# Kernel tuning notes

Hardware: AMD Instinct MI355X
Metric: run time of the kernel (lower is better)

## Reference

```python
import jax, jax.numpy as jnp
import numpy as np

DIM = 1024
NUM_EXPERTS = 8
TOP_K = 2
HIDDEN = DIM * 2
B, S = 2, 4096


def setup_inputs() -> dict:
    key = jax.random.key(0)
    ks = jax.random.split(key, 8)
    sd = 1.0 / np.sqrt(DIM)
    sh = 1.0 / np.sqrt(HIDDEN)
    return {
        "x": jax.random.normal(ks[0], (B, S, DIM), dtype=jnp.float32),
        "gate_w": jax.random.uniform(ks[1], (NUM_EXPERTS, DIM), jnp.float32, -sd, sd),
        "gate_b": jax.random.uniform(ks[2], (NUM_EXPERTS,), jnp.float32, -sd, sd),
        "W1": jax.random.uniform(ks[3], (NUM_EXPERTS, DIM, HIDDEN), jnp.float32, -sd, sd),
        "b1": jax.random.uniform(ks[4], (NUM_EXPERTS, HIDDEN), jnp.float32, -sd, sd),
        "W2": jax.random.uniform(ks[5], (NUM_EXPERTS, HIDDEN, DIM), jnp.float32, -sh, sh),
        "b2": jax.random.uniform(ks[6], (NUM_EXPERTS, DIM), jnp.float32, -sh, sh),
    }


def reference(x, gate_w, gate_b, W1, b1, W2, b2):
    Bd, Sd, D = x.shape
    xf = x.reshape(-1, D)                                  # [T, D]
    T = xf.shape[0]
    logits = xf @ gate_w.T + gate_b                        # [T, E]
    weights = jax.nn.softmax(logits.astype(jnp.float32), axis=-1)
    topk_w, topk_i = jax.lax.top_k(weights, TOP_K)         # [T, K]
    topk_w = topk_w / topk_w.sum(axis=-1, keepdims=True)
    # combine weights scattered back to dense [T, E] (top-k indices are distinct)
    comb = jnp.zeros((T, NUM_EXPERTS), topk_w.dtype)
    comb = comb.at[jnp.arange(T)[:, None], topk_i].add(topk_w)
    # dense all-expert FFN (exact GELU, matching nn.GELU default)
    h = jax.nn.gelu(jnp.einsum('td,edh->eth', xf, W1) + b1[:, None, :], approximate=False)
    y = jnp.einsum('eth,ehd->etd', h, W2) + b2[:, None, :]  # [E, T, D]
    out = jnp.einsum('etd,te->td', y, comb.astype(y.dtype)).reshape(Bd, Sd, D)
    return out, logits
```

## Files before the change

### kernel.cpp

```cpp
#include <hip/hip_runtime.h>
#include <math.h>

#define T_TOK 8192
#define DIMX 1024
#define NE 8
#define HID 2048
#define NPAIR (T_TOK * 2)
#define P_PAD (NPAIR + NE * 128)
#define GATE_TPB 32

typedef __attribute__((ext_vector_type(8))) short s16x8;
typedef __attribute__((ext_vector_type(4))) float f32x4;

static __device__ __forceinline__ unsigned short f2bf(float f) {
    union { float f; unsigned u; } v; v.f = f;
    unsigned r = v.u + 0x7FFFu + ((v.u >> 16) & 1u);
    return (unsigned short)(r >> 16);
}
static __device__ __forceinline__ float bf2f(unsigned short u) {
    union { unsigned u; float f; } v; v.u = (unsigned)u << 16; return v.f;
}

static __device__ __forceinline__ float gelu_fast(float v) {
    float u2 = -1.5957691216057308f * v * (1.f + 0.044715f * v * v);
    return v * __builtin_amdgcn_rcpf(1.f + __expf(u2));
}

static __device__ __forceinline__ void gload16(const unsigned short* g, unsigned short* l) {
    __builtin_amdgcn_global_load_lds(
        (const __attribute__((address_space(1))) unsigned int*)g,
        (__attribute__((address_space(3))) unsigned int*)l, 16, 0, 0);
}

__global__ __launch_bounds__(256) void conv_transpose2_kernel(
    const float* __restrict__ W1, const float* __restrict__ W2,
    unsigned short* __restrict__ W1t, unsigned short* __restrict__ W2t, int* counts) {
    __shared__ float tile[64][65];
    int z = blockIdx.z;
    int e = z & 7;
    if (z == 0 && blockIdx.x == 0 && blockIdx.y == 0 && threadIdx.x < NE)
        counts[threadIdx.x] = 0;
    const float* srcb; unsigned short* dstb; int R, C;
    if (z < 8) { srcb = W1; dstb = W1t; R = DIMX; C = HID; }
    else       { srcb = W2; dstb = W2t; R = HID; C = DIMX; }
    int r0 = blockIdx.y * 64, c0 = blockIdx.x * 64;
    if (r0 >= R || c0 >= C) return;
    const float* s = srcb + (size_t)e * R * C;
    unsigned short* d = dstb + (size_t)e * R * C;
    int tid = threadIdx.x;
    int lr = tid >> 4, lc4 = (tid & 15) * 4;
    #pragma unroll
    for (int it = 0; it < 4; it++) {
        float4 v = *(const float4*)&s[(size_t)(r0 + it * 16 + lr) * C + c0 + lc4];
        tile[it * 16 + lr][lc4 + 0] = v.x;
        tile[it * 16 + lr][lc4 + 1] = v.y;
        tile[it * 16 + lr][lc4 + 2] = v.z;
        tile[it * 16 + lr][lc4 + 3] = v.w;
    }
    __syncthreads();
    int cc = tid >> 3, rch = (tid & 7) * 8;
    #pragma unroll
    for (int it = 0; it < 2; it++) {
        int c = it * 32 + cc;
        unsigned short r[8];
        #pragma unroll
        for (int j = 0; j < 8; j++) r[j] = f2bf(tile[rch + j][c]);
        *(uint4*)&d[(size_t)(c0 + c) * R + r0 + rch] = *(const uint4*)&r[0];
    }
}

__global__ __launch_bounds__(256) void gate_kernel(
    const float* __restrict__ x, const float* __restrict__ gw, const float* __restrict__ gb,
    float* __restrict__ logits_out, int* counts, int* __restrict__ pair_epos,
    float* __restrict__ pair_w, unsigned short* __restrict__ xb) {
    __shared__ float sgw[NE * DIMX];
    __shared__ int lcount[NE], lbase[NE];
    __shared__ int s_e[GATE_TPB * 2];
    __shared__ int s_lp[GATE_TPB * 2];
    __shared__ float s_wv[GATE_TPB * 2];
    int tid = threadIdx.x;
    for (int i = tid; i < NE * DIMX / 4; i += 256)
        ((float4*)sgw)[i] = ((const float4*)gw)[i];
    if (tid < NE) lcount[tid] = 0;
    __syncthreads();

    int wave = tid >> 6, lane = tid & 63;
    int tbase = blockIdx.x * GATE_TPB;
    for (int r = 0; r < GATE_TPB / 4; ++r) {
        int ti = wave * (GATE_TPB / 4) + r;
        int t = tbase + ti;
        const float* xr = x + (size_t)t * DIMX;
        float acc[NE] = {};
        #pragma unroll
        for (int i = 0; i < DIMX / 256; i++) {
            float4 xv = *(const float4*)&xr[i * 256 + lane * 4];
            unsigned short rb[4] = { f2bf(xv.x), f2bf(xv.y), f2bf(xv.z), f2bf(xv.w) };
            *(uint2*)&xb[(size_t)t * DIMX + i * 256 + lane * 4] = *(const uint2*)&rb[0];
            #pragma unroll
            for (int e = 0; e < NE; e++) {
                float4 wv = *(const float4*)&sgw[e * DIMX + i * 256 + lane * 4];
                acc[e] += xv.x * wv.x + xv.y * wv.y + xv.z * wv.z + xv.w * wv.w;
            }
        }
        #pragma unroll
        for (int e = 0; e < NE; e++) {
            #pragma unroll
            for (int off = 32; off; off >>= 1) acc[e] += __shfl_xor(acc[e], off);
        }
        if (lane == 0) {
            float* lo = logits_out + (size_t)t * NE;
            #pragma unroll
            for (int e = 0; e < NE; e++) { acc[e] += gb[e]; lo[e] = acc[e]; }
            float l0 = acc[0]; int e0 = 0;
            #pragma unroll
            for (int e = 1; e < NE; e++) if (acc[e] > l0) { l0 = acc[e]; e0 = e; }
            float l1 = -1e30f; int e1 = -1;
            #pragma unroll
            for (int e = 0; e < NE; e++) if (e != e0 && acc[e] > l1) { l1 = acc[e]; e1 = e; }
            float q = expf(l1 - l0);
            float wn0 = 1.f / (1.f + q);
            float wn1 = q / (1.f + q);
            int lp0 = atomicAdd(&lcount[e0], 1);
            int lp1 = atomicAdd(&lcount[e1], 1);
            s_e[ti * 2] = e0; s_lp[ti * 2] = lp0; s_wv[ti * 2] = wn0;
            s_e[ti * 2 + 1] = e1; s_lp[ti * 2 + 1] = lp1; s_wv[ti * 2 + 1] = wn1;
        }
    }
    __syncthreads();
    if (tid < NE) lbase[tid] = atomicAdd(&counts[tid], lcount[tid]);
    __syncthreads();
    if (tid < GATE_TPB * 2) {
        int e = s_e[tid];
        int gp = lbase[e] + s_lp[tid];
        int gi = (tbase + (tid >> 1)) * 2 + (tid & 1);
        pair_epos[gi] = (e << 28) | gp;
        pair_w[gi] = s_wv[tid];
    }
}

__global__ __launch_bounds__(256) void place_kernel(
    const int* __restrict__ pair_epos, const float* __restrict__ pair_w,
    const int* __restrict__ counts, int* __restrict__ offsets_out,
    int* __restrict__ slot_token, float* __restrict__ slot_weight,
    int* __restrict__ tok2slot) {
    __shared__ int soff[NE + 1];
    __shared__ int scnt[NE];
    int tid = threadIdx.x;
    if (tid == 0) {
        int o = 0;
        soff[0] = 0;
        for (int e = 0; e < NE; e++) {
            int c = counts[e];
            scnt[e] = c;
            o += (c + 127) & ~127;
            soff[e + 1] = o;
        }
    }
    __syncthreads();
    if (blockIdx.x == 0 && tid <= NE) offsets_out[tid] = soff[tid];

    int gtid = blockIdx.x * 256 + tid;
    {
        int gbase = 0;
        #pragma unroll
        for (int e = 0; e < NE; e++) {
            int gs = soff[e] + scnt[e];
            int gl = soff[e + 1] - gs;
            int idx = gtid - gbase;
            if (idx >= 0 && idx < gl) {
                slot_token[gs + idx] = 0;
                slot_weight[gs + idx] = 0.f;
            }
            gbase += gl;
        }
    }
    int p = gtid;
    if (p >= NPAIR) return;
    int ep = pair_epos[p];
    int e = ep >> 28;
    int pos = ep & 0x0FFFFFFF;
    int slot = soff[e] + pos;
    slot_token[slot] = p >> 1;
    slot_weight[slot] = pair_w[p];
    tok2slot[p] = slot;
}

#define BARRIER() asm volatile("s_barrier" ::: "memory")
#define WAIT_VM(n) asm volatile("s_waitcnt vmcnt(" #n ")" ::: "memory")
#define WAIT_LGKM0() do { asm volatile("s_waitcnt lgkmcnt(0)" ::: "memory"); \
                          __builtin_amdgcn_sched_barrier(0); } while (0)


__global__ __launch_bounds__(512, 4) void gemm1_kernel(
    const unsigned short* __restrict__ xb, const unsigned short* __restrict__ W1t,
    const float* __restrict__ b1, const int* __restrict__ offsets,
    const int* __restrict__ slot_token, unsigned short* __restrict__ hbuf) {
    int e = blockIdx.x;
    int row_base = offsets[e];
    int rows = offsets[e + 1] - row_base;
    int m0 = blockIdx.z * 128;
    if (m0 >= rows) return;
    int n0 = blockIdx.y * 128;

    __shared__ unsigned short sA[2][128 * 64];
    __shared__ unsigned short sB[2][128 * 64];

    int tid = threadIdx.x;
    const unsigned short* w1e = W1t + (size_t)e * HID * DIMX;

    int srow = tid >> 3;
    int kperm = (tid & 7) ^ (srow & 7);
    int tok0 = slot_token[row_base + m0 + srow];
    int tok1 = slot_token[row_base + m0 + srow + 64];
    const unsigned short* gA0 = xb + (size_t)tok0 * DIMX + kperm * 8;
    const unsigned short* gA1 = xb + (size_t)tok1 * DIMX + kperm * 8;
    const unsigned short* gB0 = w1e + (size_t)(n0 + srow) * DIMX + kperm * 8;
    const unsigned short* gB1 = w1e + (size_t)(n0 + srow + 64) * DIMX + kperm * 8;

#define STG1(b, k0) do { \
        gload16(gA0 + (k0), &sA[b][tid * 8]); \
        gload16(gA1 + (k0), &sA[b][(tid + 512) * 8]); \
        gload16(gB0 + (k0), &sB[b][tid * 8]); \
        gload16(gB1 + (k0), &sB[b][(tid + 512) * 8]); \
    } while (0)

    f32x4 acc[4][2] = {};
    int wid = tid >> 6; int wr = wid >> 2, wc = wid & 3;
    int lane = tid & 63; int lr = lane & 15, lg = lane >> 4;
    int kx0 = lg ^ (lr & 7);

#define CMP1(CUR) do { \
        _Pragma("unroll") \
        for (int kk = 0; kk < 2; kk++) { \
            int kxo = (kx0 ^ (kk * 4)) * 8; \
            s16x8 af[4], bfr[2]; \
            _Pragma("unroll") \
            for (int m = 0; m < 4; m++) af[m] = *(const s16x8*)&sA[CUR][(wr * 64 + m * 16 + lr) * 64 + kxo]; \
            _Pragma("unroll") \
            for (int n = 0; n < 2; n++) bfr[n] = *(const s16x8*)&sB[CUR][(wc * 32 + n * 16 + lr) * 64 + kxo]; \
            __builtin_amdgcn_s_setprio(1); \
            _Pragma("unroll") \
            for (int m = 0; m < 4; m++) { \
                _Pragma("unroll") \
                for (int n = 0; n < 2; n++) \
                    acc[m][n] = __builtin_amdgcn_mfma_f32_16x16x32_bf16(af[m], bfr[n], acc[m][n], 0, 0, 0); \
            } \
            __builtin_amdgcn_s_setprio(0); \
        } \
    } while (0)

    const int NT = DIMX / 64;
    STG1(0, 0);
    int cur = 0;
    for (int t = 0; t < NT - 1; ++t) {
        STG1(cur ^ 1, (t + 1) * 64);
        WAIT_VM(4);
        BARRIER();
        CMP1(cur);
        WAIT_LGKM0();
        BARRIER();
        cur ^= 1;
    }
    WAIT_VM(0);
    BARRIER();
    CMP1(cur);
#undef STG1
#undef CMP1

    #pragma unroll
    for (int m = 0; m < 4; m++) {
        #pragma unroll
        for (int n = 0; n < 2; n++) {
            int col = n0 + wc * 32 + n * 16 + lr;
            float bias = b1[e * HID + col];
            #pragma unroll
            for (int i = 0; i < 4; i++) {
                int row = wr * 64 + m * 16 + lg * 4 + i;
                float v = gelu_fast(acc[m][n][i] + bias);
                hbuf[(size_t)(row_base + m0 + row) * HID + col] = f2bf(v);
            }
        }
    }
}

__global__ __launch_bounds__(512, 4) void gemm2_kernel(
    const unsigned short* __restrict__ hbuf, const unsigned short* __restrict__ W2t,
    const float* __restrict__ b2, const int* __restrict__ offsets,
    const float* __restrict__ slot_weight, unsigned short* __restrict__ ybuf) {
    int e = blockIdx.x;
    int row_base = offsets[e];
    int rows = offsets[e + 1] - row_base;
    int m0 = blockIdx.z * 128;
    if (m0 >= rows) return;
    int n0 = blockIdx.y * 128;

    __shared__ unsigned short sA[2][128 * 64];
    __shared__ unsigned short sB[2][128 * 64];
    __shared__ float s_w[128];

    int tid = threadIdx.x;
    if (tid < 128) s_w[tid] = slot_weight[row_base + m0 + tid];

    const unsigned short* ha = hbuf + (size_t)(row_base + m0) * HID;
    const unsigned short* w2e = W2t + (size_t)e * DIMX * HID;

    int srow = tid >> 3;
    int kperm = (tid & 7) ^ (srow & 7);
    const unsigned short* gA0 = ha + (size_t)srow * HID + kperm * 8;
    const unsigned short* gA1 = ha + (size_t)(srow + 64) * HID + kperm * 8;
    const unsigned short* gB0 = w2e + (size_t)(n0 + srow) * HID + kperm * 8;
    const unsigned short* gB1 = w2e + (size_t)(n0 + srow + 64) * HID + kperm * 8;

#define STG2(b, k0) do { \
        gload16(gA0 + (k0), &sA[b][tid * 8]); \
        gload16(gA1 + (k0), &sA[b][(tid + 512) * 8]); \
        gload16(gB0 + (k0), &sB[b][tid * 8]); \
        gload16(gB1 + (k0), &sB[b][(tid + 512) * 8]); \
    } while (0)

    f32x4 acc[4][2] = {};
    int wid = tid >> 6; int wr = wid >> 2, wc = wid & 3;
    int lane = tid & 63; int lr = lane & 15, lg = lane >> 4;
    int kx0 = lg ^ (lr & 7);

#define CMP2(CUR) do { \
        _Pragma("unroll") \
        for (int kk = 0; kk < 2; kk++) { \
            int kxo = (kx0 ^ (kk * 4)) * 8; \
            s16x8 af[4], bfr[2]; \
            _Pragma("unroll") \
            for (int m = 0; m < 4; m++) af[m] = *(const s16x8*)&sA[CUR][(wr * 64 + m * 16 + lr) * 64 + kxo]; \
            _Pragma("unroll") \
            for (int n = 0; n < 2; n++) bfr[n] = *(const s16x8*)&sB[CUR][(wc * 32 + n * 16 + lr) * 64 + kxo]; \
            __builtin_amdgcn_s_setprio(1); \
            _Pragma("unroll") \
            for (int m = 0; m < 4; m++) { \
                _Pragma("unroll") \
                for (int n = 0; n < 2; n++) \
                    acc[m][n] = __builtin_amdgcn_mfma_f32_16x16x32_bf16(af[m], bfr[n], acc[m][n], 0, 0, 0); \
            } \
            __builtin_amdgcn_s_setprio(0); \
        } \
    } while (0)

    const int NT = HID / 64;
    STG2(0, 0);
    int cur = 0;
    for (int t = 0; t < NT - 1; ++t) {
        STG2(cur ^ 1, (t + 1) * 64);
        WAIT_VM(4);
        BARRIER();
        CMP2(cur);
        WAIT_LGKM0();
        BARRIER();
        cur ^= 1;
    }
    WAIT_VM(0);
    BARRIER();
    CMP2(cur);
#undef STG2
#undef CMP2

    #pragma unroll
    for (int m = 0; m < 4; m++) {
        #pragma unroll
        for (int n = 0; n < 2; n++) {
            int col = n0 + wc * 32 + n * 16 + lr;
            float bias = b2[e * DIMX + col];
            #pragma unroll
            for (int i = 0; i < 4; i++) {
                int row = wr * 64 + m * 16 + lg * 4 + i;
                float v = (acc[m][n][i] + bias) * s_w[row];
                ybuf[(size_t)(row_base + m0 + row) * DIMX + col] = f2bf(v);
            }
        }
    }
}

__global__ __launch_bounds__(256) void combine_kernel(
    const unsigned short* __restrict__ ybuf, const int* __restrict__ tok2slot,
    float* __restrict__ out) {
    int t = blockIdx.x;
    int d = threadIdx.x * 4;
    int sa = tok2slot[t * 2], sb = tok2slot[t * 2 + 1];
    ushort4 a = *(const ushort4*)&ybuf[(size_t)sa * DIMX + d];
    ushort4 b = *(const ushort4*)&ybuf[(size_t)sb * DIMX + d];
    float4 o;
    o.x = bf2f(a.x) + bf2f(b.x);
    o.y = bf2f(a.y) + bf2f(b.y);
    o.z = bf2f(a.z) + bf2f(b.z);
    o.w = bf2f(a.w) + bf2f(b.w);
    *(float4*)&out[(size_t)t * DIMX + d] = o;
}

extern "C" void kernel_launch(void* const* d_in, const int* in_sizes, int n_in,
                              void* d_out, int out_size, void* d_ws, size_t ws_size,
                              hipStream_t stream) {
    const float* x  = (const float*)d_in[0];
    const float* gw = (const float*)d_in[1];
    const float* gb = (const float*)d_in[2];
    const float* W1 = (const float*)d_in[3];
    const float* b1 = (const float*)d_in[4];
    const float* W2 = (const float*)d_in[5];
    const float* b2 = (const float*)d_in[6];
    float* out = (float*)d_out;
    float* logits = out + (size_t)T_TOK * DIMX;

    char* ws = (char*)d_ws;
    unsigned short* W2t = (unsigned short*)ws; ws += (size_t)NE * DIMX * HID * 2;
    unsigned short* W1t = (unsigned short*)ws;
    unsigned short* ybuf = (unsigned short*)ws; ws += (size_t)NE * DIMX * HID * 2;
    unsigned short* xb = (unsigned short*)ws; ws += (size_t)T_TOK * DIMX * 2;
    unsigned short* hbuf = (unsigned short*)ws; ws += (size_t)P_PAD * HID * 2;
    int* counts = (int*)ws; ws += 256;
    int* offsets = (int*)ws; ws += 256;
    int* pair_epos = (int*)ws; ws += (size_t)NPAIR * 4;
    float* pair_w = (float*)ws; ws += (size_t)NPAIR * 4;
    int* slot_token = (int*)ws; ws += (size_t)P_PAD * 4;
    float* slot_weight = (float*)ws; ws += (size_t)P_PAD * 4;
    int* tok2slot = (int*)ws; ws += (size_t)NPAIR * 4;

    conv_transpose2_kernel<<<dim3(32, 32, 16), 256, 0, stream>>>(W1, W2, W1t, W2t, counts);
    gate_kernel<<<T_TOK / GATE_TPB, 256, 0, stream>>>(x, gw, gb, logits, counts, pair_epos,
                                                      pair_w, xb);
    place_kernel<<<NPAIR / 256, 256, 0, stream>>>(pair_epos, pair_w, counts, offsets,
                                                  slot_token, slot_weight, tok2slot);
    gemm1_kernel<<<dim3(NE, HID / 128, 128), 512, 0, stream>>>(xb, W1t, b1, offsets, slot_token, hbuf);
    gemm2_kernel<<<dim3(NE, DIMX / 128, 128), 512, 0, stream>>>(hbuf, W2t, b2, offsets, slot_weight, ybuf);
    combine_kernel<<<T_TOK, 256, 0, stream>>>(ybuf, tok2slot, out);
}
```

Baseline: 268.0 us.

## Merge weight transpose and gating into one prep kernel with per-block count scan

Folds the weight convert/transpose kernel and the gating kernel into a single launch, with blocks split by index and shared memory held in a union. The global atomic counter is replaced by per-block expert counts written to memory. The place kernel then computes the offsets with a shared-memory prefix scan, which makes slot assignment deterministic. This drops one launch and lets gating overlap with the transpose, at the cost of every place block redoing the 256x8 scan.

```diff
diff --git a/kernel.cpp b/kernel.cpp
--- a/kernel.cpp
+++ b/kernel.cpp
@@ -8,6 +8,7 @@
 #define NPAIR (T_TOK * 2)
 #define P_PAD (NPAIR + NE * 128)
 #define GATE_TPB 32
+#define NGATE (T_TOK / GATE_TPB)
 
 typedef __attribute__((ext_vector_type(8))) short s16x8;
 typedef __attribute__((ext_vector_type(4))) float f32x4;
@@ -32,129 +33,153 @@
         (__attribute__((address_space(3))) unsigned int*)l, 16, 0, 0);
 }
 
-__global__ __launch_bounds__(256) void conv_transpose2_kernel(
+union PrepSmem {
+    struct {
+        float sgw[NE * DIMX];
+        int lcount[NE];
+        int s_e[GATE_TPB * 2];
+        int s_lp[GATE_TPB * 2];
+        float s_wv[GATE_TPB * 2];
+    } g;
+    float tile[64][65];
+};
+
+__global__ __launch_bounds__(256) void prep_kernel(
+    const float* __restrict__ x, const float* __restrict__ gw, const float* __restrict__ gb,
     const float* __restrict__ W1, const float* __restrict__ W2,
-    unsigned short* __restrict__ W1t, unsigned short* __restrict__ W2t, int* counts) {
-    __shared__ float tile[64][65];
-    int z = blockIdx.z;
-    int e = z & 7;
-    if (z == 0 && blockIdx.x == 0 && blockIdx.y == 0 && threadIdx.x < NE)
-        counts[threadIdx.x] = 0;
-    const float* srcb; unsigned short* dstb; int R, C;
-    if (z < 8) { srcb = W1; dstb = W1t; R = DIMX; C = HID; }
-    else       { srcb = W2; dstb = W2t; R = HID; C = DIMX; }
-    int r0 = blockIdx.y * 64, c0 = blockIdx.x * 64;
-    if (r0 >= R || c0 >= C) return;
-    const float* s = srcb + (size_t)e * R * C;
-    unsigned short* d = dstb + (size_t)e * R * C;
+    float* __restrict__ logits_out, int* __restrict__ blk_counts,
+    int* __restrict__ pair_epos, float* __restrict__ pair_w,
+    unsigned short* __restrict__ xb, unsigned short* __restrict__ W1t,
+    unsigned short* __restrict__ W2t) {
+    __shared__ PrepSmem sm;
+    int bid = blockIdx.x;
     int tid = threadIdx.x;
-    int lr = tid >> 4, lc4 = (tid & 15) * 4;
-    #pragma unroll
-    for (int it = 0; it < 4; it++) {
-        float4 v = *(const float4*)&s[(size_t)(r0 + it * 16 + lr) * C + c0 + lc4];
-        tile[it * 16 + lr][lc4 + 0] = v.x;
-        tile[it * 16 + lr][lc4 + 1] = v.y;
-        tile[it * 16 + lr][lc4 + 2] = v.z;
-        tile[it * 16 + lr][lc4 + 3] = v.w;
-    }
-    __syncthreads();
-    int cc = tid >> 3, rch = (tid & 7) * 8;
-    #pragma unroll
-    for (int it = 0; it < 2; it++) {
-        int c = it * 32 + cc;
-        unsigned short r[8];
-        #pragma unroll
-        for (int j = 0; j < 8; j++) r[j] = f2bf(tile[rch + j][c]);
-        *(uint4*)&d[(size_t)(c0 + c) * R + r0 + rch] = *(const uint4*)&r[0];
-    }
-}
-
-__global__ __launch_bounds__(256) void gate_kernel(
-    const float* __restrict__ x, const float* __restrict__ gw, const float* __restrict__ gb,
-    float* __restrict__ logits_out, int* counts, int* __restrict__ pair_epos,
-    float* __restrict__ pair_w, unsigned short* __restrict__ xb) {
-    __shared__ float sgw[NE * DIMX];
-    __shared__ int lcount[NE], lbase[NE];
-    __shared__ int s_e[GATE_TPB * 2];
-    __shared__ int s_lp[GATE_TPB * 2];
-    __shared__ float s_wv[GATE_TPB * 2];
-    int tid = threadIdx.x;
-    for (int i = tid; i < NE * DIMX / 4; i += 256)
-        ((float4*)sgw)[i] = ((const float4*)gw)[i];
-    if (tid < NE) lcount[tid] = 0;
-    __syncthreads();
-
-    int wave = tid >> 6, lane = tid & 63;
-    int tbase = blockIdx.x * GATE_TPB;
-    for (int r = 0; r < GATE_TPB / 4; ++r) {
-        int ti = wave * (GATE_TPB / 4) + r;
-        int t = tbase + ti;
-        const float* xr = x + (size_t)t * DIMX;
-        float acc[NE] = {};
-        #pragma unroll
-        for (int i = 0; i < DIMX / 256; i++) {
-            float4 xv = *(const float4*)&xr[i * 256 + lane * 4];
-            unsigned short rb[4] = { f2bf(xv.x), f2bf(xv.y), f2bf(xv.z), f2bf(xv.w) };
-            *(uint2*)&xb[(size_t)t * DIMX + i * 256 + lane * 4] = *(const uint2*)&rb[0];
+
+    if (bid < NGATE) {
+        for (int i = tid; i < NE * DIMX / 4; i += 256)
+            ((float4*)sm.g.sgw)[i] = ((const float4*)gw)[i];
+        if (tid < NE) sm.g.lcount[tid] = 0;
+        __syncthreads();
+
+        int wave = tid >> 6, lane = tid & 63;
+        int tbase = bid * GATE_TPB;
+        for (int r = 0; r < GATE_TPB / 4; ++r) {
+            int ti = wave * (GATE_TPB / 4) + r;
+            int t = tbase + ti;
+            const float* xr = x + (size_t)t * DIMX;
+            float acc[NE] = {};
+            #pragma unroll
+            for (int i = 0; i < DIMX / 256; i++) {
+                float4 xv = *(const float4*)&xr[i * 256 + lane * 4];
+                unsigned short rb[4] = { f2bf(xv.x), f2bf(xv.y), f2bf(xv.z), f2bf(xv.w) };
+                *(uint2*)&xb[(size_t)t * DIMX + i * 256 + lane * 4] = *(const uint2*)&rb[0];
+                #pragma unroll
+                for (int e = 0; e < NE; e++) {
+                    float4 wv = *(const float4*)&sm.g.sgw[e * DIMX + i * 256 + lane * 4];
+                    acc[e] += xv.x * wv.x + xv.y * wv.y + xv.z * wv.z + xv.w * wv.w;
+                }
+            }
             #pragma unroll
             for (int e = 0; e < NE; e++) {
-                float4 wv = *(const float4*)&sgw[e * DIMX + i * 256 + lane * 4];
-                acc[e] += xv.x * wv.x + xv.y * wv.y + xv.z * wv.z + xv.w * wv.w;
-            }
-        }
-        #pragma unroll
-        for (int e = 0; e < NE; e++) {
+                #pragma unroll
+                for (int off = 32; off; off >>= 1) acc[e] += __shfl_xor(acc[e], off);
+            }
+            if (lane == 0) {
+                float* lo = logits_out + (size_t)t * NE;
+                #pragma unroll
+                for (int e = 0; e < NE; e++) { acc[e] += gb[e]; lo[e] = acc[e]; }
+                float l0 = acc[0]; int e0 = 0;
+                #pragma unroll
+                for (int e = 1; e < NE; e++) if (acc[e] > l0) { l0 = acc[e]; e0 = e; }
+                float l1 = -1e30f; int e1 = -1;
+                #pragma unroll
+                for (int e = 0; e < NE; e++) if (e != e0 && acc[e] > l1) { l1 = acc[e]; e1 = e; }
+                float q = expf(l1 - l0);
+                float wn0 = 1.f / (1.f + q);
+                float wn1 = q / (1.f + q);
+                int lp0 = atomicAdd(&sm.g.lcount[e0], 1);
+                int lp1 = atomicAdd(&sm.g.lcount[e1], 1);
+                sm.g.s_e[ti * 2] = e0; sm.g.s_lp[ti * 2] = lp0; sm.g.s_wv[ti * 2] = wn0;
+                sm.g.s_e[ti * 2 + 1] = e1; sm.g.s_lp[ti * 2 + 1] = lp1; sm.g.s_wv[ti * 2 + 1] = wn1;
+            }
+        }
+        __syncthreads();
+        if (tid < NE) blk_counts[bid * NE + tid] = sm.g.lcount[tid];
+        if (tid < GATE_TPB * 2) {
+            int gi = (tbase + (tid >> 1)) * 2 + (tid & 1);
+            pair_epos[gi] = (sm.g.s_e[tid] << 28) | sm.g.s_lp[tid];
+            pair_w[gi] = sm.g.s_wv[tid];
+        }
+    } else {
+        int zb = bid - NGATE;
+        int z = zb >> 10;
+        int rem = zb & 1023;
+        int by = rem >> 5, bx = rem & 31;
+        int e = z & 7;
+        const float* srcb; unsigned short* dstb; int R, C;
+        if (z < 8) { srcb = W1; dstb = W1t; R = DIMX; C = HID; }
+        else       { srcb = W2; dstb = W2t; R = HID; C = DIMX; }
+        int r0 = by * 64, c0 = bx * 64;
+        if (r0 >= R || c0 >= C) return;
+        const float* s = srcb + (size_t)e * R * C;
+        unsigned short* d = dstb + (size_t)e * R * C;
+        int lr = tid >> 4, lc4 = (tid & 15) * 4;
+        #pragma unroll
+        for (int it = 0; it < 4; it++) {
+            float4 v = *(const float4*)&s[(size_t)(r0 + it * 16 + lr) * C + c0 + lc4];
+            sm.tile[it * 16 + lr][lc4 + 0] = v.x;
+            sm.tile[it * 16 + lr][lc4 + 1] = v.y;
+            sm.tile[it * 16 + lr][lc4 + 2] = v.z;
+            sm.tile[it * 16 + lr][lc4 + 3] = v.w;
+        }
+        __syncthreads();
+        int cc = tid >> 3, rch = (tid & 7) * 8;
+        #pragma unroll
+        for (int it = 0; it < 2; it++) {
+            int c = it * 32 + cc;
+            unsigned short r[8];
             #pragma unroll
-            for (int off = 32; off; off >>= 1) acc[e] += __shfl_xor(acc[e], off);
-        }
-        if (lane == 0) {
-            float* lo = logits_out + (size_t)t * NE;
-            #pragma unroll
-            for (int e = 0; e < NE; e++) { acc[e] += gb[e]; lo[e] = acc[e]; }
-            float l0 = acc[0]; int e0 = 0;
-            #pragma unroll
-            for (int e = 1; e < NE; e++) if (acc[e] > l0) { l0 = acc[e]; e0 = e; }
-            float l1 = -1e30f; int e1 = -1;
-            #pragma unroll
-            for (int e = 0; e < NE; e++) if (e != e0 && acc[e] > l1) { l1 = acc[e]; e1 = e; }
-            float q = expf(l1 - l0);
-            float wn0 = 1.f / (1.f + q);
-            float wn1 = q / (1.f + q);
-            int lp0 = atomicAdd(&lcount[e0], 1);
-            int lp1 = atomicAdd(&lcount[e1], 1);
-            s_e[ti * 2] = e0; s_lp[ti * 2] = lp0; s_wv[ti * 2] = wn0;
-            s_e[ti * 2 + 1] = e1; s_lp[ti * 2 + 1] = lp1; s_wv[ti * 2 + 1] = wn1;
-        }
-    }
-    __syncthreads();
-    if (tid < NE) lbase[tid] = atomicAdd(&counts[tid], lcount[tid]);
-    __syncthreads();
-    if (tid < GATE_TPB * 2) {
-        int e = s_e[tid];
-        int gp = lbase[e] + s_lp[tid];
-        int gi = (tbase + (tid >> 1)) * 2 + (tid & 1);
-        pair_epos[gi] = (e << 28) | gp;
-        pair_w[gi] = s_wv[tid];
+            for (int j = 0; j < 8; j++) r[j] = f2bf(sm.tile[rch + j][c]);
+            *(uint4*)&d[(size_t)(c0 + c) * R + r0 + rch] = *(const uint4*)&r[0];
+        }
     }
 }
 
 __global__ __launch_bounds__(256) void place_kernel(
     const int* __restrict__ pair_epos, const float* __restrict__ pair_w,
-    const int* __restrict__ counts, int* __restrict__ offsets_out,
+    const int* __restrict__ blk_counts, int* __restrict__ offsets_out,
     int* __restrict__ slot_token, float* __restrict__ slot_weight,
     int* __restrict__ tok2slot) {
+    __shared__ int scnt[NGATE][NE];
+    __shared__ int sbase[NGATE][NE];
     __shared__ int soff[NE + 1];
-    __shared__ int scnt[NE];
+    __shared__ int stot[NE];
     int tid = threadIdx.x;
+    #pragma unroll
+    for (int e = 0; e < NE; e++) scnt[tid][e] = blk_counts[tid * NE + e];
+    __syncthreads();
+    {
+        int e = tid >> 5, j = tid & 31;
+        int cs[8];
+        int part = 0;
+        #pragma unroll
+        for (int i = 0; i < 8; i++) { cs[i] = part; part += scnt[j * 8 + i][e]; }
+        int inc = part;
+        #pragma unroll
+        for (int d = 1; d < 32; d <<= 1) {
+            int up = __shfl_up(inc, d, 32);
+            if (j >= d) inc += up;
+        }
+        int excl = inc - part;
+        #pragma unroll
+        for (int i = 0; i < 8; i++) sbase[j * 8 + i][e] = excl + cs[i];
+        if (j == 31) stot[e] = inc;
+    }
+    __syncthreads();
     if (tid == 0) {
         int o = 0;
         soff[0] = 0;
-        for (int e = 0; e < NE; e++) {
-            int c = counts[e];
-            scnt[e] = c;
-            o += (c + 127) & ~127;
-            soff[e + 1] = o;
-        }
+        for (int k = 0; k < NE; k++) { o += (stot[k] + 127) & ~127; soff[k + 1] = o; }
     }
     __syncthreads();
     if (blockIdx.x == 0 && tid <= NE) offsets_out[tid] = soff[tid];
@@ -163,9 +188,9 @@
     {
         int gbase = 0;
         #pragma unroll
-        for (int e = 0; e < NE; e++) {
-            int gs = soff[e] + scnt[e];
-            int gl = soff[e + 1] - gs;
+        for (int k = 0; k < NE; k++) {
+            int gs = soff[k] + stot[k];
+            int gl = soff[k + 1] - gs;
             int idx = gtid - gbase;
             if (idx >= 0 && idx < gl) {
                 slot_token[gs + idx] = 0;
@@ -175,11 +200,11 @@
         }
     }
     int p = gtid;
-    if (p >= NPAIR) return;
     int ep = pair_epos[p];
-    int e = ep >> 28;
-    int pos = ep & 0x0FFFFFFF;
-    int slot = soff[e] + pos;
+    int pe = ep >> 28;
+    int lp = ep & 0x0FFFFFFF;
+    int g = p >> 6;
+    int slot = soff[pe] + sbase[g][pe] + lp;
     slot_token[slot] = p >> 1;
     slot_weight[slot] = pair_w[p];
     tok2slot[p] = slot;
@@ -412,7 +437,7 @@
     unsigned short* ybuf = (unsigned short*)ws; ws += (size_t)NE * DIMX * HID * 2;
     unsigned short* xb = (unsigned short*)ws; ws += (size_t)T_TOK * DIMX * 2;
     unsigned short* hbuf = (unsigned short*)ws; ws += (size_t)P_PAD * HID * 2;
-    int* counts = (int*)ws; ws += 256;
+    int* blk_counts = (int*)ws; ws += (size_t)NGATE * NE * 4;
     int* offsets = (int*)ws; ws += 256;
     int* pair_epos = (int*)ws; ws += (size_t)NPAIR * 4;
     float* pair_w = (float*)ws; ws += (size_t)NPAIR * 4;
@@ -420,10 +445,9 @@
     float* slot_weight = (float*)ws; ws += (size_t)P_PAD * 4;
     int* tok2slot = (int*)ws; ws += (size_t)NPAIR * 4;
 
-    conv_transpose2_kernel<<<dim3(32, 32, 16), 256, 0, stream>>>(W1, W2, W1t, W2t, counts);
-    gate_kernel<<<T_TOK / GATE_TPB, 256, 0, stream>>>(x, gw, gb, logits, counts, pair_epos,
-                                                      pair_w, xb);
-    place_kernel<<<NPAIR / 256, 256, 0, stream>>>(pair_epos, pair_w, counts, offsets,
+    prep_kernel<<<NGATE + 16384, 256, 0, stream>>>(x, gw, gb, W1, W2, logits, blk_counts,
+                                                   pair_epos, pair_w, xb, W1t, W2t);
+    place_kernel<<<NPAIR / 256, 256, 0, stream>>>(pair_epos, pair_w, blk_counts, offsets,
                                                   slot_token, slot_weight, tok2slot);
     gemm1_kernel<<<dim3(NE, HID / 128, 128), 512, 0, stream>>>(xb, W1t, b1, offsets, slot_token, hbuf);
     gemm2_kernel<<<dim3(NE, DIMX / 128, 128), 512, 0, stream>>>(hbuf, W2t, b2, offsets, slot_weight, ybuf);
```

Measured after the change: 257.7 us. 3.9% less time.
